# Optimization experiments

Measured on AMD Instinct MI355X. Metric: run time of the kernel, lower is better.

The kernel has to match this reference:

```python
import jax, jax.numpy as jnp
import numpy as np

N, M, K, CIN, COUT = 65536, 16385, 16, 256, 512
RATIO = 0.25
LN_EPS = 1e-5


def setup_inputs() -> dict:
    key = jax.random.key(0)
    k0, k1, k2, k3, k4 = jax.random.split(key, 5)
    xyz = jax.random.normal(k0, (N, 3), dtype=jnp.float32)
    feats = jax.random.normal(k1, (N, CIN), dtype=jnp.float32)
    samp_idx = jax.random.randint(k2, (M,), 0, N, dtype=jnp.int32)
    knn_idx = jax.random.randint(k3, (M, K), 0, N, dtype=jnp.int32)
    norm_w = jnp.ones((CIN,), dtype=jnp.float32)
    norm_b = jnp.zeros((CIN,), dtype=jnp.float32)
    lin_w = jax.random.normal(k4, (COUT, CIN), dtype=jnp.float32) * (1.0 / np.sqrt(CIN))
    return {"xyz": xyz, "feats": feats, "norm_w": norm_w, "norm_b": norm_b,
            "lin_w": lin_w, "samp_idx": samp_idx, "knn_idx": knn_idx, "offset": N}


def reference(xyz, feats, norm_w, norm_b, lin_w, samp_idx, knn_idx, offset):
    # n_offset = int(offset * ratio) + 1 (single point cloud)
    m = int(offset * RATIO) + 1
    n_offset = jnp.array([m], dtype=jnp.int32)
    # FPS output -> sampled coordinates
    n_xyz = xyz[samp_idx]                                  # [m, 3]
    # queryandgroup(use_xyz=False): gather k-NN neighbor features
    g = feats[knn_idx]                                     # [m, k, cin]
    # LayerNorm over channel dim
    mu = jnp.mean(g, axis=-1, keepdims=True)
    var = jnp.mean(jnp.square(g - mu), axis=-1, keepdims=True)
    normed = (g - mu) * jax.lax.rsqrt(var + LN_EPS) * norm_w + norm_b
    # bias-free Linear cin -> cout
    proj = jnp.einsum('mkc,oc->mko', normed, lin_w)        # [m, k, cout]
    # MaxPool1d over the k neighbors
    out = jnp.max(proj, axis=1)                            # [m, cout]
    return n_xyz, out, n_offset
```

## Files before the change

kernel.cpp:

```cpp
#include <hip/hip_runtime.h>

#define M_PTS   16385
#define K_NB    16
#define CIN_C   256
#define COUT_C  512
#define N_ROWS  65536
#define LN_EPS  1e-5f

#define OUT_XYZ_ELEMS (M_PTS * 3)
#define OUT_FEAT_OFF  OUT_XYZ_ELEMS
#define OUT_NOFF_IDX  (OUT_XYZ_ELEMS + M_PTS * COUT_C)

#define LN_BLOCKS   (N_ROWS / 4)
#define PREP_BLOCKS 512

#define NBLK 513
#define PPB  32

#define B_SCALE 16.0f
#define B_INV   0.0625f

#define AROW_B 272

typedef __attribute__((ext_vector_type(4))) float f32x4;

__device__ __forceinline__ float wave_sum64(float v) {
  v += __int_as_float(__builtin_amdgcn_update_dpp(0, __float_as_int(v), 0xB1, 0xF, 0xF, false));
  v += __int_as_float(__builtin_amdgcn_update_dpp(0, __float_as_int(v), 0x4E, 0xF, 0xF, false));
  v += __int_as_float(__builtin_amdgcn_update_dpp(0, __float_as_int(v), 0x141, 0xF, 0xF, false));
  v += __int_as_float(__builtin_amdgcn_update_dpp(0, __float_as_int(v), 0x140, 0xF, 0xF, false));
  v += __int_as_float(__builtin_amdgcn_update_dpp(0, __float_as_int(v), 0x142, 0xA, 0xF, false));
  v += __int_as_float(__builtin_amdgcn_update_dpp(0, __float_as_int(v), 0x143, 0xC, 0xF, false));
  return __int_as_float(__builtin_amdgcn_readlane(__float_as_int(v), 63));
}

__device__ __forceinline__ int ln_pack(float4 g, float4 nw, float4 nb) {
  float s1 = (g.x + g.y) + (g.z + g.w);
  float s2 = g.x * g.x + g.y * g.y + g.z * g.z + g.w * g.w;
  float S1 = wave_sum64(s1);
  float S2 = wave_sum64(s2);
  float mu  = S1 * (1.0f / 256.0f);
  float var = fmaf(-mu, mu, S2 * (1.0f / 256.0f));
  float rs  = rsqrtf(var + LN_EPS);
  float a = fmaf((g.x - mu) * rs, nw.x, nb.x);
  float b = fmaf((g.y - mu) * rs, nw.y, nb.y);
  float c = fmaf((g.z - mu) * rs, nw.z, nb.z);
  float d = fmaf((g.w - mu) * rs, nw.w, nb.w);
  int v = __builtin_amdgcn_cvt_pk_fp8_f32(a, b, 0, false);
  v = __builtin_amdgcn_cvt_pk_fp8_f32(c, d, v, true);
  return v;
}

__device__ __forceinline__ int wdw_of(int lane) {
  return ((lane >> 4) << 6) + (((lane >> 1) & 3) << 4)
       + (lane & 8) + ((lane & 1) << 2);
}

__global__ void prep_kernel(const float* __restrict__ lin_w,
                            const float* __restrict__ xyz,
                            const float* __restrict__ feats,
                            const float* __restrict__ norm_w,
                            const float* __restrict__ norm_b,
                            const int*   __restrict__ samp_idx,
                            const int*   __restrict__ offset,
                            unsigned char* __restrict__ lw8,
                            unsigned char* __restrict__ tab,
                            float*  __restrict__ out) {
  int bx = blockIdx.x;
  if (bx < LN_BLOCKS) {
    int lane = threadIdx.x & 63;
    int row  = (bx << 2) + (threadIdx.x >> 6);
    float4 g  = ((const float4*)(feats + (size_t)row * CIN_C))[lane];
    float4 nw = ((const float4*)norm_w)[lane];
    float4 nb = ((const float4*)norm_b)[lane];
    int pk = ln_pack(g, nw, nb);
    *(int*)(tab + ((size_t)row << 8) + wdw_of(lane)) = pk;
    return;
  }
  int tid = (bx - LN_BLOCKS) * 256 + threadIdx.x;
  if (tid < COUT_C * CIN_C) {
    int o = tid >> 8;
    int c = tid & 255;
    int pos = ((o >> 5) << 13) | (((o >> 4) & 1) << 12) | ((c >> 5) << 9)
            | ((((c >> 3) & 3) * 16 + (o & 15)) << 3) | (c & 7);
    int pk = __builtin_amdgcn_cvt_pk_fp8_f32(lin_w[tid] * B_SCALE, 0.0f, 0, false);
    lw8[pos] = (unsigned char)(pk & 0xFF);
  }
  if (tid < OUT_XYZ_ELEMS) {
    int p = tid / 3;
    int c = tid - p * 3;
    out[tid] = xyz[(size_t)samp_idx[p] * 3 + c];
  }
  if (tid == 0) out[OUT_NOFF_IDX] = (float)(offset[0] / 4 + 1);
}

__device__ __forceinline__ void load_row(const unsigned char* __restrict__ tab,
                                         int idx, unsigned char* ldsrow, int lane) {
  const unsigned char* src = tab + ((size_t)(unsigned)idx << 8) + (lane << 2);
  __builtin_amdgcn_global_load_lds(
      (const __attribute__((address_space(1))) unsigned int*)src,
      (__attribute__((address_space(3))) unsigned int*)ldsrow,
      4, 0, 0);
}

__device__ __forceinline__ void gemm_pool(const unsigned char* rowbase,
                                          const long Breg[8][2], int quad,
                                          float& v0, float& v1) {
  ulonglong2 q0 = *(const ulonglong2*)(rowbase + 0   + quad * 16);
  ulonglong2 q1 = *(const ulonglong2*)(rowbase + 64  + quad * 16);
  ulonglong2 q2 = *(const ulonglong2*)(rowbase + 128 + quad * 16);
  ulonglong2 q3 = *(const ulonglong2*)(rowbase + 192 + quad * 16);
  f32x4 a0 = {0.f, 0.f, 0.f, 0.f}, a1 = {0.f, 0.f, 0.f, 0.f};
  a0 = __builtin_amdgcn_mfma_f32_16x16x32_fp8_fp8((long)q0.x, Breg[0][0], a0, 0, 0, 0);
  a1 = __builtin_amdgcn_mfma_f32_16x16x32_fp8_fp8((long)q0.x, Breg[0][1], a1, 0, 0, 0);
  a0 = __builtin_amdgcn_mfma_f32_16x16x32_fp8_fp8((long)q0.y, Breg[1][0], a0, 0, 0, 0);
  a1 = __builtin_amdgcn_mfma_f32_16x16x32_fp8_fp8((long)q0.y, Breg[1][1], a1, 0, 0, 0);
  a0 = __builtin_amdgcn_mfma_f32_16x16x32_fp8_fp8((long)q1.x, Breg[2][0], a0, 0, 0, 0);
  a1 = __builtin_amdgcn_mfma_f32_16x16x32_fp8_fp8((long)q1.x, Breg[2][1], a1, 0, 0, 0);
  a0 = __builtin_amdgcn_mfma_f32_16x16x32_fp8_fp8((long)q1.y, Breg[3][0], a0, 0, 0, 0);
  a1 = __builtin_amdgcn_mfma_f32_16x16x32_fp8_fp8((long)q1.y, Breg[3][1], a1, 0, 0, 0);
  a0 = __builtin_amdgcn_mfma_f32_16x16x32_fp8_fp8((long)q2.x, Breg[4][0], a0, 0, 0, 0);
  a1 = __builtin_amdgcn_mfma_f32_16x16x32_fp8_fp8((long)q2.x, Breg[4][1], a1, 0, 0, 0);
  a0 = __builtin_amdgcn_mfma_f32_16x16x32_fp8_fp8((long)q2.y, Breg[5][0], a0, 0, 0, 0);
  a1 = __builtin_amdgcn_mfma_f32_16x16x32_fp8_fp8((long)q2.y, Breg[5][1], a1, 0, 0, 0);
  a0 = __builtin_amdgcn_mfma_f32_16x16x32_fp8_fp8((long)q3.x, Breg[6][0], a0, 0, 0, 0);
  a1 = __builtin_amdgcn_mfma_f32_16x16x32_fp8_fp8((long)q3.x, Breg[6][1], a1, 0, 0, 0);
  a0 = __builtin_amdgcn_mfma_f32_16x16x32_fp8_fp8((long)q3.y, Breg[7][0], a0, 0, 0, 0);
  a1 = __builtin_amdgcn_mfma_f32_16x16x32_fp8_fp8((long)q3.y, Breg[7][1], a1, 0, 0, 0);
  v0 = fmaxf(fmaxf(a0[0], a0[1]), fmaxf(a0[2], a0[3]));
  v0 = fmaxf(v0, __shfl_xor(v0, 16, 64));
  v0 = fmaxf(v0, __shfl_xor(v0, 32, 64));
  v1 = fmaxf(fmaxf(a1[0], a1[1]), fmaxf(a1[2], a1[3]));
  v1 = fmaxf(v1, __shfl_xor(v1, 16, 64));
  v1 = fmaxf(v1, __shfl_xor(v1, 32, 64));
}

__global__ __launch_bounds__(1024, 8)
void td_main(const unsigned char* __restrict__ tab,
             const unsigned char* __restrict__ lw8,
             const int*    __restrict__ knn,
             float* __restrict__ out) {
  __shared__ __align__(16) unsigned char A8[4][2][16][AROW_B];
  __shared__ int Kidx[PPB * K_NB];

  const int tid  = threadIdx.x;
  const int lane = tid & 63;
  const int w    = tid >> 6;
  const int quad = lane >> 4;
  const int lcol = lane & 15;

  const int pstart = blockIdx.x * PPB;
  const int npts   = min(pstart + PPB, M_PTS) - pstart;
  if (npts <= 0) return;

  for (int i = tid; i < npts * K_NB; i += 1024)
    Kidx[i] = knn[pstart * K_NB + i];

  long Breg[8][2];
  {
    const unsigned char* base = lw8 + (w << 13) + lane * 8;
#pragma unroll
    for (int g = 0; g < 2; ++g)
#pragma unroll
      for (int kk = 0; kk < 8; ++kk) {
        Breg[kk][g] = *(const long*)(base + (g << 12) + (kk << 9));
        asm volatile("" : "+v"(Breg[kk][g]));
      }
  }

  __syncthreads();

  load_row(tab, Kidx[w],                                &A8[0][0][w][0], lane);
  load_row(tab, Kidx[min(1, npts - 1) * K_NB + w],      &A8[0][1][w][0], lane);

  const int nit = (npts + 1) >> 1;
  for (int it = 0; it < nit; ++it) {
    const int pa = 2 * it, pb = 2 * it + 1;

    if (it + 1 < nit) {
      int qa = min(pa + 2, npts - 1), qb = min(pa + 3, npts - 1);
      int b = (it + 1) & 3;
      load_row(tab, Kidx[qa * K_NB + w], &A8[b][0][w][0], lane);
      load_row(tab, Kidx[qb * K_NB + w], &A8[b][1][w][0], lane);
    }

    if (it == 0) {
      if (nit > 1) asm volatile("s_waitcnt vmcnt(2)" ::: "memory");
      else         asm volatile("s_waitcnt vmcnt(0)" ::: "memory");
    } else if (it + 1 < nit) {
      asm volatile("s_waitcnt vmcnt(4)" ::: "memory");
    } else {
      asm volatile("s_waitcnt vmcnt(2)" ::: "memory");
    }
    __builtin_amdgcn_s_barrier();

    const unsigned char* Ab = &A8[it & 3][0][0][0];

    float v0, v1;
    gemm_pool(Ab + lcol * AROW_B, Breg, quad, v0, v1);
    float* outa = out + OUT_FEAT_OFF + (size_t)(pstart + pa) * COUT_C + w * 32;
    if (quad < 2) outa[quad * 16 + lcol] = (quad ? v1 : v0) * B_INV;

    gemm_pool(Ab + (16 + lcol) * AROW_B, Breg, quad, v0, v1);
    if (pb < npts) {
      float* outb = out + OUT_FEAT_OFF + (size_t)(pstart + pb) * COUT_C + w * 32;
      if (quad < 2) outb[quad * 16 + lcol] = (quad ? v1 : v0) * B_INV;
    }
  }
}

extern "C" void kernel_launch(void* const* d_in, const int* in_sizes, int n_in,
                              void* d_out, int out_size, void* d_ws, size_t ws_size,
                              hipStream_t stream) {
  const float* xyz      = (const float*)d_in[0];
  const float* feats    = (const float*)d_in[1];
  const float* norm_w   = (const float*)d_in[2];
  const float* norm_b   = (const float*)d_in[3];
  const float* lin_w    = (const float*)d_in[4];
  const int*   samp_idx = (const int*)d_in[5];
  const int*   knn      = (const int*)d_in[6];
  const int*   offset   = (const int*)d_in[7];
  float* out = (float*)d_out;
  unsigned char* lw8 = (unsigned char*)d_ws;
  unsigned char* tab = (unsigned char*)d_ws + (1 << 17);

  prep_kernel<<<LN_BLOCKS + PREP_BLOCKS, 256, 0, stream>>>(
      lin_w, xyz, feats, norm_w, norm_b, samp_idx, offset, lw8, tab, out);

  td_main<<<NBLK, 1024, 0, stream>>>(tab, lw8, knn, out);
}
```

Before: 161.5 us.

## Switch pooled GEMM to 32x32x16 fp8 MFMA with permlane32 swap reduction

Replaces the two 16x16x32 fp8 MFMA chains per point pair with a single 32x32x16 fp8 MFMA chain covering both points (32 neighbor rows) and all 32 output channels per wave. The LN-packed table and the weight layout are reordered to match the 32x32 operand layout, and the max-pool over neighbors becomes an in-register reduction plus one v_permlane32_swap instead of cross-lane shuffles. This removes the shuffle-based reduction, halves the LDS A reads, and lets every lane write output rather than only half of them. Wait counts are adjusted because the direct-to-LDS loads per iteration changed. The trade-off is a larger accumulator (16 VGPRs) and a dependence on the gfx950 permlane32 instruction.

```diff
diff --git a/kernel.cpp b/kernel.cpp
--- a/kernel.cpp
+++ b/kernel.cpp
@@ -22,7 +22,8 @@
 
 #define AROW_B 272
 
-typedef __attribute__((ext_vector_type(4))) float f32x4;
+typedef __attribute__((ext_vector_type(4)))  float f32x4;
+typedef __attribute__((ext_vector_type(16))) float f32x16;
 
 __device__ __forceinline__ float wave_sum64(float v) {
   v += __int_as_float(__builtin_amdgcn_update_dpp(0, __float_as_int(v), 0xB1, 0xF, 0xF, false));
@@ -51,9 +52,8 @@
   return v;
 }
 
-__device__ __forceinline__ int wdw_of(int lane) {
-  return ((lane >> 4) << 6) + (((lane >> 1) & 3) << 4)
-       + (lane & 8) + ((lane & 1) << 2);
+__device__ __forceinline__ int wdw32_of(int lane) {
+  return (((lane >> 1) & 1) << 7) | ((lane >> 2) << 3) | ((lane & 1) << 2);
 }
 
 __global__ void prep_kernel(const float* __restrict__ lin_w,
@@ -74,15 +74,15 @@
     float4 nw = ((const float4*)norm_w)[lane];
     float4 nb = ((const float4*)norm_b)[lane];
     int pk = ln_pack(g, nw, nb);
-    *(int*)(tab + ((size_t)row << 8) + wdw_of(lane)) = pk;
+    *(int*)(tab + ((size_t)row << 8) + wdw32_of(lane)) = pk;
     return;
   }
   int tid = (bx - LN_BLOCKS) * 256 + threadIdx.x;
   if (tid < COUT_C * CIN_C) {
     int o = tid >> 8;
     int c = tid & 255;
-    int pos = ((o >> 5) << 13) | (((o >> 4) & 1) << 12) | ((c >> 5) << 9)
-            | ((((c >> 3) & 3) * 16 + (o & 15)) << 3) | (c & 7);
+    int pos = ((o >> 5) << 13) | ((c >> 4) << 9)
+            | (((((c >> 3) & 1) << 5) | (o & 31)) << 3) | (c & 7);
     int pk = __builtin_amdgcn_cvt_pk_fp8_f32(lin_w[tid] * B_SCALE, 0.0f, 0, false);
     lw8[pos] = (unsigned char)(pk & 0xFF);
   }
@@ -103,51 +103,19 @@
       4, 0, 0);
 }
 
-__device__ __forceinline__ void gemm_pool(const unsigned char* rowbase,
-                                          const long Breg[8][2], int quad,
-                                          float& v0, float& v1) {
-  ulonglong2 q0 = *(const ulonglong2*)(rowbase + 0   + quad * 16);
-  ulonglong2 q1 = *(const ulonglong2*)(rowbase + 64  + quad * 16);
-  ulonglong2 q2 = *(const ulonglong2*)(rowbase + 128 + quad * 16);
-  ulonglong2 q3 = *(const ulonglong2*)(rowbase + 192 + quad * 16);
-  f32x4 a0 = {0.f, 0.f, 0.f, 0.f}, a1 = {0.f, 0.f, 0.f, 0.f};
-  a0 = __builtin_amdgcn_mfma_f32_16x16x32_fp8_fp8((long)q0.x, Breg[0][0], a0, 0, 0, 0);
-  a1 = __builtin_amdgcn_mfma_f32_16x16x32_fp8_fp8((long)q0.x, Breg[0][1], a1, 0, 0, 0);
-  a0 = __builtin_amdgcn_mfma_f32_16x16x32_fp8_fp8((long)q0.y, Breg[1][0], a0, 0, 0, 0);
-  a1 = __builtin_amdgcn_mfma_f32_16x16x32_fp8_fp8((long)q0.y, Breg[1][1], a1, 0, 0, 0);
-  a0 = __builtin_amdgcn_mfma_f32_16x16x32_fp8_fp8((long)q1.x, Breg[2][0], a0, 0, 0, 0);
-  a1 = __builtin_amdgcn_mfma_f32_16x16x32_fp8_fp8((long)q1.x, Breg[2][1], a1, 0, 0, 0);
-  a0 = __builtin_amdgcn_mfma_f32_16x16x32_fp8_fp8((long)q1.y, Breg[3][0], a0, 0, 0, 0);
-  a1 = __builtin_amdgcn_mfma_f32_16x16x32_fp8_fp8((long)q1.y, Breg[3][1], a1, 0, 0, 0);
-  a0 = __builtin_amdgcn_mfma_f32_16x16x32_fp8_fp8((long)q2.x, Breg[4][0], a0, 0, 0, 0);
-  a1 = __builtin_amdgcn_mfma_f32_16x16x32_fp8_fp8((long)q2.x, Breg[4][1], a1, 0, 0, 0);
-  a0 = __builtin_amdgcn_mfma_f32_16x16x32_fp8_fp8((long)q2.y, Breg[5][0], a0, 0, 0, 0);
-  a1 = __builtin_amdgcn_mfma_f32_16x16x32_fp8_fp8((long)q2.y, Breg[5][1], a1, 0, 0, 0);
-  a0 = __builtin_amdgcn_mfma_f32_16x16x32_fp8_fp8((long)q3.x, Breg[6][0], a0, 0, 0, 0);
-  a1 = __builtin_amdgcn_mfma_f32_16x16x32_fp8_fp8((long)q3.x, Breg[6][1], a1, 0, 0, 0);
-  a0 = __builtin_amdgcn_mfma_f32_16x16x32_fp8_fp8((long)q3.y, Breg[7][0], a0, 0, 0, 0);
-  a1 = __builtin_amdgcn_mfma_f32_16x16x32_fp8_fp8((long)q3.y, Breg[7][1], a1, 0, 0, 0);
-  v0 = fmaxf(fmaxf(a0[0], a0[1]), fmaxf(a0[2], a0[3]));
-  v0 = fmaxf(v0, __shfl_xor(v0, 16, 64));
-  v0 = fmaxf(v0, __shfl_xor(v0, 32, 64));
-  v1 = fmaxf(fmaxf(a1[0], a1[1]), fmaxf(a1[2], a1[3]));
-  v1 = fmaxf(v1, __shfl_xor(v1, 16, 64));
-  v1 = fmaxf(v1, __shfl_xor(v1, 32, 64));
-}
-
 __global__ __launch_bounds__(1024, 8)
 void td_main(const unsigned char* __restrict__ tab,
              const unsigned char* __restrict__ lw8,
              const int*    __restrict__ knn,
              float* __restrict__ out) {
-  __shared__ __align__(16) unsigned char A8[4][2][16][AROW_B];
+  __shared__ __align__(16) unsigned char A8[4][32][AROW_B];
   __shared__ int Kidx[PPB * K_NB];
 
   const int tid  = threadIdx.x;
   const int lane = tid & 63;
   const int w    = tid >> 6;
-  const int quad = lane >> 4;
-  const int lcol = lane & 15;
+  const int half = lane >> 5;
+  const int r32  = lane & 31;
 
   const int pstart = blockIdx.x * PPB;
   const int npts   = min(pstart + PPB, M_PTS) - pstart;
@@ -156,22 +124,22 @@
   for (int i = tid; i < npts * K_NB; i += 1024)
     Kidx[i] = knn[pstart * K_NB + i];
 
-  long Breg[8][2];
+  long Breg[16];
   {
     const unsigned char* base = lw8 + (w << 13) + lane * 8;
 #pragma unroll
-    for (int g = 0; g < 2; ++g)
-#pragma unroll
-      for (int kk = 0; kk < 8; ++kk) {
-        Breg[kk][g] = *(const long*)(base + (g << 12) + (kk << 9));
-        asm volatile("" : "+v"(Breg[kk][g]));
-      }
+    for (int kk = 0; kk < 16; ++kk) {
+      Breg[kk] = *(const long*)(base + (kk << 9));
+      asm volatile("" : "+v"(Breg[kk]));
+    }
   }
 
   __syncthreads();
 
-  load_row(tab, Kidx[w],                                &A8[0][0][w][0], lane);
-  load_row(tab, Kidx[min(1, npts - 1) * K_NB + w],      &A8[0][1][w][0], lane);
+  load_row(tab, Kidx[w],                           &A8[0][w][0],      lane);
+  load_row(tab, Kidx[min(1, npts - 1) * K_NB + w], &A8[0][16 + w][0], lane);
+
+  float* const outbase = out + OUT_FEAT_OFF + (size_t)pstart * COUT_C + w * 32 + r32;
 
   const int nit = (npts + 1) >> 1;
   for (int it = 0; it < nit; ++it) {
@@ -180,32 +148,41 @@
     if (it + 1 < nit) {
       int qa = min(pa + 2, npts - 1), qb = min(pa + 3, npts - 1);
       int b = (it + 1) & 3;
-      load_row(tab, Kidx[qa * K_NB + w], &A8[b][0][w][0], lane);
-      load_row(tab, Kidx[qb * K_NB + w], &A8[b][1][w][0], lane);
+      load_row(tab, Kidx[qa * K_NB + w], &A8[b][w][0],      lane);
+      load_row(tab, Kidx[qb * K_NB + w], &A8[b][16 + w][0], lane);
     }
 
     if (it == 0) {
       if (nit > 1) asm volatile("s_waitcnt vmcnt(2)" ::: "memory");
       else         asm volatile("s_waitcnt vmcnt(0)" ::: "memory");
     } else if (it + 1 < nit) {
-      asm volatile("s_waitcnt vmcnt(4)" ::: "memory");
+      asm volatile("s_waitcnt vmcnt(3)" ::: "memory");
     } else {
-      asm volatile("s_waitcnt vmcnt(2)" ::: "memory");
+      asm volatile("s_waitcnt vmcnt(1)" ::: "memory");
     }
     __builtin_amdgcn_s_barrier();
 
-    const unsigned char* Ab = &A8[it & 3][0][0][0];
-
-    float v0, v1;
-    gemm_pool(Ab + lcol * AROW_B, Breg, quad, v0, v1);
-    float* outa = out + OUT_FEAT_OFF + (size_t)(pstart + pa) * COUT_C + w * 32;
-    if (quad < 2) outa[quad * 16 + lcol] = (quad ? v1 : v0) * B_INV;
-
-    gemm_pool(Ab + (16 + lcol) * AROW_B, Breg, quad, v0, v1);
-    if (pb < npts) {
-      float* outb = out + OUT_FEAT_OFF + (size_t)(pstart + pb) * COUT_C + w * 32;
-      if (quad < 2) outb[quad * 16 + lcol] = (quad ? v1 : v0) * B_INV;
-    }
+    const unsigned char* rowb = &A8[it & 3][r32][0] + (half << 7);
+
+    f32x16 acc = {0.f, 0.f, 0.f, 0.f, 0.f, 0.f, 0.f, 0.f,
+                  0.f, 0.f, 0.f, 0.f, 0.f, 0.f, 0.f, 0.f};
+#pragma unroll
+    for (int t = 0; t < 8; ++t) {
+      ulonglong2 q = *(const ulonglong2*)(rowb + t * 16);
+      acc = __builtin_amdgcn_mfma_f32_32x32x16_fp8_fp8((long)q.x, Breg[2 * t],     acc, 0, 0, 0);
+      acc = __builtin_amdgcn_mfma_f32_32x32x16_fp8_fp8((long)q.y, Breg[2 * t + 1], acc, 0, 0, 0);
+    }
+
+    float ra = fmaxf(fmaxf(fmaxf(acc[0], acc[1]),  fmaxf(acc[2],  acc[3])),
+                     fmaxf(fmaxf(acc[4], acc[5]),  fmaxf(acc[6],  acc[7])));
+    float rb = fmaxf(fmaxf(fmaxf(acc[8], acc[9]),  fmaxf(acc[10], acc[11])),
+                     fmaxf(fmaxf(acc[12], acc[13]), fmaxf(acc[14], acc[15])));
+    int ia = __float_as_int(ra), ib = __float_as_int(rb);
+    asm volatile("v_permlane32_swap_b32 %0, %1" : "+v"(ia), "+v"(ib));
+    float v = fmaxf(__int_as_float(ia), __int_as_float(ib)) * B_INV;
+
+    int pt = pa + half;
+    if (pt < npts) outbase[(size_t)pt * COUT_C] = v;
   }
 }
 
```

Measured after the change: 166.3 us. 1.03x slower.

## Give each wave 64 output channels using 8 waves per block and permlane-swap max reduction

Applied to the files above, without the earlier changes.

Each wave now computes 64 output columns (four MFMA accumulator chains) instead of 32, so blocks drop from 16 to 8 waves and the weight layout is reorganised to match. Each A row loaded from LDS feeds four MFMAs instead of two, which halves LDS read traffic per output, and every lane stores a useful output instead of half the lanes idling. The cross-quad max uses v_permlane16/32_swap in place of shfl_xor. In exchange, each thread holds twice as many weight registers and there are fewer waves to hide gather latency.

```diff
diff --git a/kernel.cpp b/kernel.cpp
--- a/kernel.cpp
+++ b/kernel.cpp
@@ -81,8 +81,8 @@
   if (tid < COUT_C * CIN_C) {
     int o = tid >> 8;
     int c = tid & 255;
-    int pos = ((o >> 5) << 13) | (((o >> 4) & 1) << 12) | ((c >> 5) << 9)
-            | ((((c >> 3) & 3) * 16 + (o & 15)) << 3) | (c & 7);
+    int pos = ((o >> 6) << 14) | (((o >> 4) & 3) << 12) | ((c >> 5) << 9)
+            | (((((c >> 3) & 3) << 4) | (o & 15)) << 3) | (c & 7);
     int pk = __builtin_amdgcn_cvt_pk_fp8_f32(lin_w[tid] * B_SCALE, 0.0f, 0, false);
     lw8[pos] = (unsigned char)(pk & 0xFF);
   }
@@ -103,44 +103,45 @@
       4, 0, 0);
 }
 
-__device__ __forceinline__ void gemm_pool(const unsigned char* rowbase,
-                                          const long Breg[8][2], int quad,
-                                          float& v0, float& v1) {
+__device__ __forceinline__ float quadmax(float v) {
+  int a = __float_as_int(v), b = __float_as_int(v);
+  asm volatile("v_permlane16_swap_b32 %0, %1" : "+v"(a), "+v"(b));
+  float m = fmaxf(__int_as_float(a), __int_as_float(b));
+  int c = __float_as_int(m), d = __float_as_int(m);
+  asm volatile("v_permlane32_swap_b32 %0, %1" : "+v"(c), "+v"(d));
+  return fmaxf(__int_as_float(c), __int_as_float(d));
+}
+
+__device__ __forceinline__ float gemm_pool64(const unsigned char* rowbase,
+                                             const long Breg[8][4], int quad) {
   ulonglong2 q0 = *(const ulonglong2*)(rowbase + 0   + quad * 16);
   ulonglong2 q1 = *(const ulonglong2*)(rowbase + 64  + quad * 16);
   ulonglong2 q2 = *(const ulonglong2*)(rowbase + 128 + quad * 16);
   ulonglong2 q3 = *(const ulonglong2*)(rowbase + 192 + quad * 16);
-  f32x4 a0 = {0.f, 0.f, 0.f, 0.f}, a1 = {0.f, 0.f, 0.f, 0.f};
-  a0 = __builtin_amdgcn_mfma_f32_16x16x32_fp8_fp8((long)q0.x, Breg[0][0], a0, 0, 0, 0);
-  a1 = __builtin_amdgcn_mfma_f32_16x16x32_fp8_fp8((long)q0.x, Breg[0][1], a1, 0, 0, 0);
-  a0 = __builtin_amdgcn_mfma_f32_16x16x32_fp8_fp8((long)q0.y, Breg[1][0], a0, 0, 0, 0);
-  a1 = __builtin_amdgcn_mfma_f32_16x16x32_fp8_fp8((long)q0.y, Breg[1][1], a1, 0, 0, 0);
-  a0 = __builtin_amdgcn_mfma_f32_16x16x32_fp8_fp8((long)q1.x, Breg[2][0], a0, 0, 0, 0);
-  a1 = __builtin_amdgcn_mfma_f32_16x16x32_fp8_fp8((long)q1.x, Breg[2][1], a1, 0, 0, 0);
-  a0 = __builtin_amdgcn_mfma_f32_16x16x32_fp8_fp8((long)q1.y, Breg[3][0], a0, 0, 0, 0);
-  a1 = __builtin_amdgcn_mfma_f32_16x16x32_fp8_fp8((long)q1.y, Breg[3][1], a1, 0, 0, 0);
-  a0 = __builtin_amdgcn_mfma_f32_16x16x32_fp8_fp8((long)q2.x, Breg[4][0], a0, 0, 0, 0);
-  a1 = __builtin_amdgcn_mfma_f32_16x16x32_fp8_fp8((long)q2.x, Breg[4][1], a1, 0, 0, 0);
-  a0 = __builtin_amdgcn_mfma_f32_16x16x32_fp8_fp8((long)q2.y, Breg[5][0], a0, 0, 0, 0);
-  a1 = __builtin_amdgcn_mfma_f32_16x16x32_fp8_fp8((long)q2.y, Breg[5][1], a1, 0, 0, 0);
-  a0 = __builtin_amdgcn_mfma_f32_16x16x32_fp8_fp8((long)q3.x, Breg[6][0], a0, 0, 0, 0);
-  a1 = __builtin_amdgcn_mfma_f32_16x16x32_fp8_fp8((long)q3.x, Breg[6][1], a1, 0, 0, 0);
-  a0 = __builtin_amdgcn_mfma_f32_16x16x32_fp8_fp8((long)q3.y, Breg[7][0], a0, 0, 0, 0);
-  a1 = __builtin_amdgcn_mfma_f32_16x16x32_fp8_fp8((long)q3.y, Breg[7][1], a1, 0, 0, 0);
-  v0 = fmaxf(fmaxf(a0[0], a0[1]), fmaxf(a0[2], a0[3]));
-  v0 = fmaxf(v0, __shfl_xor(v0, 16, 64));
-  v0 = fmaxf(v0, __shfl_xor(v0, 32, 64));
-  v1 = fmaxf(fmaxf(a1[0], a1[1]), fmaxf(a1[2], a1[3]));
-  v1 = fmaxf(v1, __shfl_xor(v1, 16, 64));
-  v1 = fmaxf(v1, __shfl_xor(v1, 32, 64));
-}
-
-__global__ __launch_bounds__(1024, 8)
+  f32x4 a0 = {0.f,0.f,0.f,0.f}, a1 = {0.f,0.f,0.f,0.f};
+  f32x4 a2 = {0.f,0.f,0.f,0.f}, a3 = {0.f,0.f,0.f,0.f};
+#define MF4(Aop, kk)                                                          \
+  a0 = __builtin_amdgcn_mfma_f32_16x16x32_fp8_fp8((long)(Aop), Breg[kk][0], a0, 0, 0, 0); \
+  a1 = __builtin_amdgcn_mfma_f32_16x16x32_fp8_fp8((long)(Aop), Breg[kk][1], a1, 0, 0, 0); \
+  a2 = __builtin_amdgcn_mfma_f32_16x16x32_fp8_fp8((long)(Aop), Breg[kk][2], a2, 0, 0, 0); \
+  a3 = __builtin_amdgcn_mfma_f32_16x16x32_fp8_fp8((long)(Aop), Breg[kk][3], a3, 0, 0, 0);
+  MF4(q0.x, 0) MF4(q0.y, 1) MF4(q1.x, 2) MF4(q1.y, 3)
+  MF4(q2.x, 4) MF4(q2.y, 5) MF4(q3.x, 6) MF4(q3.y, 7)
+#undef MF4
+  float v0 = quadmax(fmaxf(fmaxf(a0[0], a0[1]), fmaxf(a0[2], a0[3])));
+  float v1 = quadmax(fmaxf(fmaxf(a1[0], a1[1]), fmaxf(a1[2], a1[3])));
+  float v2 = quadmax(fmaxf(fmaxf(a2[0], a2[1]), fmaxf(a2[2], a2[3])));
+  float v3 = quadmax(fmaxf(fmaxf(a3[0], a3[1]), fmaxf(a3[2], a3[3])));
+  float sv = (quad == 0) ? v0 : (quad == 1) ? v1 : (quad == 2) ? v2 : v3;
+  return sv * B_INV;
+}
+
+__global__ __launch_bounds__(512, 4)
 void td_main(const unsigned char* __restrict__ tab,
              const unsigned char* __restrict__ lw8,
              const int*    __restrict__ knn,
              float* __restrict__ out) {
-  __shared__ __align__(16) unsigned char A8[4][2][16][AROW_B];
+  __shared__ __align__(16) unsigned char A8[4][32][AROW_B];
   __shared__ int Kidx[PPB * K_NB];
 
   const int tid  = threadIdx.x;
@@ -153,14 +154,14 @@
   const int npts   = min(pstart + PPB, M_PTS) - pstart;
   if (npts <= 0) return;
 
-  for (int i = tid; i < npts * K_NB; i += 1024)
+  for (int i = tid; i < npts * K_NB; i += 512)
     Kidx[i] = knn[pstart * K_NB + i];
 
-  long Breg[8][2];
+  long Breg[8][4];
   {
-    const unsigned char* base = lw8 + (w << 13) + lane * 8;
+    const unsigned char* base = lw8 + (w << 14) + lane * 8;
 #pragma unroll
-    for (int g = 0; g < 2; ++g)
+    for (int g = 0; g < 4; ++g)
 #pragma unroll
       for (int kk = 0; kk < 8; ++kk) {
         Breg[kk][g] = *(const long*)(base + (g << 12) + (kk << 9));
@@ -170,8 +171,15 @@
 
   __syncthreads();
 
-  load_row(tab, Kidx[w],                                &A8[0][0][w][0], lane);
-  load_row(tab, Kidx[min(1, npts - 1) * K_NB + w],      &A8[0][1][w][0], lane);
+  {
+    int p1 = min(1, npts - 1);
+    load_row(tab, Kidx[w],                 &A8[0][w][0],      lane);
+    load_row(tab, Kidx[8 + w],             &A8[0][8 + w][0],  lane);
+    load_row(tab, Kidx[p1 * K_NB + w],     &A8[0][16 + w][0], lane);
+    load_row(tab, Kidx[p1 * K_NB + 8 + w], &A8[0][24 + w][0], lane);
+  }
+
+  float* const outbase = out + OUT_FEAT_OFF + (size_t)pstart * COUT_C + w * 64 + lane;
 
   const int nit = (npts + 1) >> 1;
   for (int it = 0; it < nit; ++it) {
@@ -180,32 +188,29 @@
     if (it + 1 < nit) {
       int qa = min(pa + 2, npts - 1), qb = min(pa + 3, npts - 1);
       int b = (it + 1) & 3;
-      load_row(tab, Kidx[qa * K_NB + w], &A8[b][0][w][0], lane);
-      load_row(tab, Kidx[qb * K_NB + w], &A8[b][1][w][0], lane);
+      load_row(tab, Kidx[qa * K_NB + w],     &A8[b][w][0],      lane);
+      load_row(tab, Kidx[qa * K_NB + 8 + w], &A8[b][8 + w][0],  lane);
+      load_row(tab, Kidx[qb * K_NB + w],     &A8[b][16 + w][0], lane);
+      load_row(tab, Kidx[qb * K_NB + 8 + w], &A8[b][24 + w][0], lane);
     }
 
     if (it == 0) {
-      if (nit > 1) asm volatile("s_waitcnt vmcnt(2)" ::: "memory");
+      if (nit > 1) asm volatile("s_waitcnt vmcnt(4)" ::: "memory");
       else         asm volatile("s_waitcnt vmcnt(0)" ::: "memory");
     } else if (it + 1 < nit) {
-      asm volatile("s_waitcnt vmcnt(4)" ::: "memory");
+      asm volatile("s_waitcnt vmcnt(6)" ::: "memory");
     } else {
       asm volatile("s_waitcnt vmcnt(2)" ::: "memory");
     }
     __builtin_amdgcn_s_barrier();
 
-    const unsigned char* Ab = &A8[it & 3][0][0][0];
-
-    float v0, v1;
-    gemm_pool(Ab + lcol * AROW_B, Breg, quad, v0, v1);
-    float* outa = out + OUT_FEAT_OFF + (size_t)(pstart + pa) * COUT_C + w * 32;
-    if (quad < 2) outa[quad * 16 + lcol] = (quad ? v1 : v0) * B_INV;
-
-    gemm_pool(Ab + (16 + lcol) * AROW_B, Breg, quad, v0, v1);
-    if (pb < npts) {
-      float* outb = out + OUT_FEAT_OFF + (size_t)(pstart + pb) * COUT_C + w * 32;
-      if (quad < 2) outb[quad * 16 + lcol] = (quad ? v1 : v0) * B_INV;
-    }
+    const unsigned char* Ab = &A8[it & 3][0][0];
+
+    float va = gemm_pool64(Ab + lcol * AROW_B, Breg, quad);
+    outbase[(size_t)pa * COUT_C] = va;
+
+    float vb = gemm_pool64(Ab + (16 + lcol) * AROW_B, Breg, quad);
+    if (pb < npts) outbase[(size_t)pb * COUT_C] = vb;
   }
 }
 
@@ -227,5 +232,5 @@
   prep_kernel<<<LN_BLOCKS + PREP_BLOCKS, 256, 0, stream>>>(
       lin_w, xyz, feats, norm_w, norm_b, samp_idx, offset, lw8, tab, out);
 
-  td_main<<<NBLK, 1024, 0, stream>>>(tab, lw8, knn, out);
-}
+  td_main<<<NBLK, 512, 0, stream>>>(tab, lw8, knn, out);
+}
```

Result: slower. 167.1 us (+3.5%).
